# Optimization experiments

Measured on AMD Instinct MI355X. Metric: run time of the kernel, lower is better.

The kernel has to match this reference:

```python
import jax, jax.numpy as jnp
import numpy as np

ROUNDS = 2
N_NODES = 50000
N_EDGES = 800000
NODE_DIM = 128
EDGE_DIM = 32
ACT_DIM = 128


def setup_inputs() -> dict:
    key = jax.random.key(0)
    ks = jax.random.split(key, 10)
    hv = jax.random.normal(ks[0], (N_NODES, NODE_DIM), dtype=jnp.float32)
    he = jax.random.normal(ks[1], (N_EDGES, EDGE_DIM), dtype=jnp.float32)
    src = jax.random.randint(ks[2], (N_EDGES,), 0, N_NODES, dtype=jnp.int32)
    dst = jax.random.randint(ks[3], (N_EDGES,), 0, N_NODES, dtype=jnp.int32)
    cat_dim = 2 * NODE_DIM + EDGE_DIM  # 288
    W_msg = jax.random.normal(ks[4], (ROUNDS, cat_dim, ACT_DIM), dtype=jnp.float32) * 0.05
    b_msg = jax.random.normal(ks[5], (ROUNDS, ACT_DIM), dtype=jnp.float32) * 0.05
    W_ih = jax.random.normal(ks[6], (ROUNDS, ACT_DIM, 3 * NODE_DIM), dtype=jnp.float32) * 0.05
    W_hh = jax.random.normal(ks[7], (ROUNDS, NODE_DIM, 3 * NODE_DIM), dtype=jnp.float32) * 0.05
    b_ih = jax.random.normal(ks[8], (ROUNDS, 3 * NODE_DIM), dtype=jnp.float32) * 0.05
    b_hh = jax.random.normal(ks[9], (ROUNDS, 3 * NODE_DIM), dtype=jnp.float32) * 0.05
    return {"hv": hv, "he": he, "src": src, "dst": dst,
            "W_msg": W_msg, "b_msg": b_msg,
            "W_ih": W_ih, "W_hh": W_hh, "b_ih": b_ih, "b_hh": b_hh}


def _gru_cell(x, h, W_ih, W_hh, b_ih, b_hh):
    # torch.nn.GRUCell math, gate order (r, z, n)
    gi = x @ W_ih + b_ih  # [N, 3H]
    gh = h @ W_hh + b_hh  # [N, 3H]
    ir, iz, in_ = jnp.split(gi, 3, axis=-1)
    hr, hz, hn = jnp.split(gh, 3, axis=-1)
    r = jax.nn.sigmoid(ir + hr)
    z = jax.nn.sigmoid(iz + hz)
    n = jnp.tanh(in_ + r * hn)
    return (1.0 - z) * n + z * h


def reference(hv, he, src, dst, W_msg, b_msg, W_ih, W_hh, b_ih, b_hh):
    N, nd = hv.shape
    for t in range(ROUNDS):
        # Linear on concat([hv_src, hv_dst, he]) == sum of block matmuls
        Ws = W_msg[t, :nd]          # src block
        Wd = W_msg[t, nd:2 * nd]    # dst block
        We = W_msg[t, 2 * nd:]      # edge block
        msg = hv[src] @ Ws + hv[dst] @ Wd + he @ We + b_msg[t]  # [E, act]
        a = jax.ops.segment_sum(msg, dst, num_segments=N)        # per-node sum over incoming edges
        hv = _gru_cell(a, hv, W_ih[t], W_hh[t], b_ih[t], b_hh[t])
    return hv
```

## Files before the change

### kernel.cpp

```cpp
#include <hip/hip_runtime.h>

#define N_NODES 50000
#define N_EDGES 800000
#define ND 128
#define ED 32
#define AD 128
#define CAT 288
#define G3 384

#define XPAD 296
#define KSTEPS 9
#define SCAN_BS 512

typedef unsigned short ushort_t;
typedef __attribute__((ext_vector_type(8))) short bfrag;
typedef __attribute__((ext_vector_type(4))) float f32x4;

__device__ __forceinline__ unsigned int f2bf(float f) {
    unsigned int u = __float_as_uint(f);
    return (u + 0x7FFFu + ((u >> 16) & 1u)) >> 16;
}
__device__ __forceinline__ void split2(float a, float b,
                                       unsigned int& hi, unsigned int& lo) {
    const unsigned int ha = f2bf(a), hb = f2bf(b);
    const float ra = a - __uint_as_float(ha << 16);
    const float rb = b - __uint_as_float(hb << 16);
    hi = ha | (hb << 16);
    lo = f2bf(ra) | (f2bf(rb) << 16);
}
__device__ __forceinline__ void split1(float a, ushort_t& hi, ushort_t& lo) {
    const unsigned int ha = f2bf(a);
    const float ra = a - __uint_as_float(ha << 16);
    hi = (ushort_t)ha;
    lo = (ushort_t)f2bf(ra);
}

__global__ __launch_bounds__(256) void hist_kernel(
    const int* __restrict__ dst, int* __restrict__ deg)
{
    const int e = blockIdx.x * 256 + threadIdx.x;
    if (e < N_EDGES) atomicAdd(&deg[dst[e]], 1);
}

__global__ __launch_bounds__(SCAN_BS) void scan_block_kernel(
    const int* __restrict__ in, int* __restrict__ out,
    int* __restrict__ bsum, int n)
{
    __shared__ int s[SCAN_BS];
    const int g = blockIdx.x * SCAN_BS + threadIdx.x;
    const int v = (g < n) ? in[g] : 0;
    s[threadIdx.x] = v;
    __syncthreads();
    for (int off = 1; off < SCAN_BS; off <<= 1) {
        const int x = (threadIdx.x >= off) ? s[threadIdx.x - off] : 0;
        __syncthreads();
        s[threadIdx.x] += x;
        __syncthreads();
    }
    if (g < n) out[g] = s[threadIdx.x] - v;
    if (threadIdx.x == SCAN_BS - 1) bsum[blockIdx.x] = s[threadIdx.x];
}

__global__ __launch_bounds__(128) void scan_sums_kernel(int* __restrict__ bsum, int nb)
{
    __shared__ int s[128];
    const int i = threadIdx.x;
    s[i] = (i < nb) ? bsum[i] : 0;
    __syncthreads();
    if (i == 0) {
        int acc = 0;
        for (int k = 0; k < nb; ++k) { const int t = s[k]; s[k] = acc; acc += t; }
    }
    __syncthreads();
    if (i < nb) bsum[i] = s[i];
}

__global__ __launch_bounds__(SCAN_BS) void scan_add_kernel(
    int* __restrict__ rowptr, int* __restrict__ cursor,
    const int* __restrict__ bsum, int n)
{
    const int g = blockIdx.x * SCAN_BS + threadIdx.x;
    if (g < n) {
        const int v = rowptr[g] + bsum[blockIdx.x];
        rowptr[g] = v;
        cursor[g] = v;
    }
}

__global__ __launch_bounds__(256) void fill_kernel(
    const int* __restrict__ dst, const int* __restrict__ src,
    int* __restrict__ cursor, int* __restrict__ perm,
    int* __restrict__ src_sorted)
{
    const int e = blockIdx.x * 256 + threadIdx.x;
    if (e < N_EDGES) {
        const int p = atomicAdd(&cursor[dst[e]], 1);
        perm[p] = e;
        src_sorted[p] = src[e];
    }
}

__global__ __launch_bounds__(256) void esum_kernel(
    const float* __restrict__ he, const int* __restrict__ perm,
    const int* __restrict__ rowptr, float* __restrict__ E)
{
    const int id = blockIdx.x * 256 + threadIdx.x;
    if (id >= N_NODES * ED) return;
    const int v = id >> 5, c = id & 31;
    const int r0 = rowptr[v], r1 = rowptr[v + 1];
    float s = 0.f;
    int i = r0;
    for (; i + 4 <= r1; i += 4) {
        const int p0 = perm[i],     p1 = perm[i + 1];
        const int p2 = perm[i + 2], p3 = perm[i + 3];
        const float a = he[(size_t)p0 * ED + c];
        const float b = he[(size_t)p1 * ED + c];
        const float d = he[(size_t)p2 * ED + c];
        const float f = he[(size_t)p3 * ED + c];
        s += (a + b) + (d + f);
    }
    for (; i < r1; ++i)
        s += he[(size_t)perm[i] * ED + c];
    E[(size_t)v * ED + c] = s;
}

__global__ __launch_bounds__(256) void convert_w_kernel(
    const float* __restrict__ W,
    ushort_t* __restrict__ Wt_hi, ushort_t* __restrict__ Wt_lo)
{
    const int id = blockIdx.x * 256 + threadIdx.x;
    if (id >= 2 * CAT * AD) return;
    const int n = id & (AD - 1);
    const int k = (id >> 7) % CAT;
    const int t = id / (CAT * AD);
    const float w = W[(size_t)t * CAT * AD + (size_t)k * AD + n];
    const unsigned int hi = f2bf(w);
    const float r = w - __uint_as_float(hi << 16);
    const size_t o = (size_t)t * AD * CAT + (size_t)n * CAT + k;
    Wt_hi[o] = (ushort_t)hi;
    Wt_lo[o] = (ushort_t)f2bf(r);
}

__global__ __launch_bounds__(256) void convert_gatew_kernel(
    const float* __restrict__ W_ih, const float* __restrict__ W_hh,
    ushort_t* __restrict__ Bih_hi, ushort_t* __restrict__ Bih_lo,
    ushort_t* __restrict__ Bhh_hi, ushort_t* __restrict__ Bhh_lo)
{
    const int id = blockIdx.x * 256 + threadIdx.x;
    if (id >= 196608) return;
    const int t   = id / 98304;
    const int rem = id % 98304;
    const int mat = rem / 49152;
    const int q   = rem % 49152;
    const int nt = q / 2048,  r1 = q % 2048;
    const int ks = r1 / 512,  r2 = r1 % 512;
    const int kq = r2 / 128,  r3 = r2 % 128;
    const int lr = r3 / 8,    j  = r3 % 8;
    const int n = nt * 16 + lr;
    const int k = ks * 32 + kq * 8 + j;
    const float* W = mat ? W_hh : W_ih;
    const float w = W[(size_t)t * ND * G3 + (size_t)k * G3 + n];
    const unsigned int hi = f2bf(w);
    const float res = w - __uint_as_float(hi << 16);
    const size_t o = (size_t)t * 49152 + q;
    if (mat) { Bhh_hi[o] = (ushort_t)hi; Bhh_lo[o] = (ushort_t)f2bf(res); }
    else     { Bih_hi[o] = (ushort_t)hi; Bih_lo[o] = (ushort_t)f2bf(res); }
}

__global__ __launch_bounds__(256) void agg_kernel(
    const float* __restrict__ hv, const int* __restrict__ src_sorted,
    const int* __restrict__ rowptr,
    ushort_t* __restrict__ S_hi, ushort_t* __restrict__ S_lo)
{
    const int v = blockIdx.x * 4 + (threadIdx.x >> 6);
    if (v >= N_NODES) return;
    const int lane = threadIdx.x & 63;
    const int r0 = rowptr[v], r1 = rowptr[v + 1];
    const float2* hv2 = (const float2*)hv;
    float sx = 0.f, sy = 0.f;
    int i = r0;
    for (; i + 8 <= r1; i += 8) {
        const int s0 = src_sorted[i],     s1 = src_sorted[i + 1];
        const int s2 = src_sorted[i + 2], s3 = src_sorted[i + 3];
        const int s4 = src_sorted[i + 4], s5 = src_sorted[i + 5];
        const int s6 = src_sorted[i + 6], s7 = src_sorted[i + 7];
        const float2 a = hv2[(size_t)s0 * 64 + lane];
        const float2 b = hv2[(size_t)s1 * 64 + lane];
        const float2 c = hv2[(size_t)s2 * 64 + lane];
        const float2 d = hv2[(size_t)s3 * 64 + lane];
        const float2 e = hv2[(size_t)s4 * 64 + lane];
        const float2 f = hv2[(size_t)s5 * 64 + lane];
        const float2 g = hv2[(size_t)s6 * 64 + lane];
        const float2 h = hv2[(size_t)s7 * 64 + lane];
        sx += ((a.x + b.x) + (c.x + d.x)) + ((e.x + f.x) + (g.x + h.x));
        sy += ((a.y + b.y) + (c.y + d.y)) + ((e.y + f.y) + (g.y + h.y));
    }
    for (; i < r1; ++i) {
        const float2 a = hv2[(size_t)src_sorted[i] * 64 + lane];
        sx += a.x; sy += a.y;
    }
    unsigned int h, l;
    split2(sx, sy, h, l);
    ((unsigned int*)S_hi)[(size_t)v * 64 + lane] = h;
    ((unsigned int*)S_lo)[(size_t)v * 64 + lane] = l;
}

__global__ __launch_bounds__(256, 2) void fused_msg_gru_kernel(
    const ushort_t* __restrict__ S_hi, const ushort_t* __restrict__ S_lo,
    const float* __restrict__ h_cur, const float* __restrict__ E,
    const int* __restrict__ rowptr,
    const ushort_t* __restrict__ Wt_hi, const ushort_t* __restrict__ Wt_lo,
    const float* __restrict__ bmsg,
    const ushort_t* __restrict__ Bih_hi, const ushort_t* __restrict__ Bih_lo,
    const ushort_t* __restrict__ Bhh_hi, const ushort_t* __restrict__ Bhh_lo,
    const float* __restrict__ b_ih, const float* __restrict__ b_hh,
    float* __restrict__ h_out)
{
    __shared__ __align__(16) char smem[67072];
    ushort_t* xh    = (ushort_t*)smem;
    ushort_t* xl    = xh + 32 * XPAD;
    ushort_t* sh_hi = xl + 32 * XPAD;
    ushort_t* sh_lo = sh_hi + 32 * 136;
    ushort_t* sa_hi = (ushort_t*)smem;
    ushort_t* sa_lo = sa_hi + 32 * 136;
    float* grz = (float*)smem;
    float* gin = grz + 32 * 260;
    float* ghn = gin + 32 * 132;
    __shared__ float sdeg[32];

    const int t    = threadIdx.x;
    const int wave = t >> 6;
    const int lane = t & 63;
    const int kq   = lane >> 4;
    const int lr   = lane & 15;
    const int n0   = blockIdx.x * 32;

    bfrag mbh[2][KSTEPS], mbl[2][KSTEPS];
    float mbias[2];
    #pragma unroll
    for (int nt = 0; nt < 2; ++nt) {
        const int n = wave * 32 + nt * 16 + lr;
        mbias[nt] = bmsg[n];
        const ushort_t* ph = Wt_hi + (size_t)n * CAT + kq * 8;
        const ushort_t* pl = Wt_lo + (size_t)n * CAT + kq * 8;
        #pragma unroll
        for (int ks = 0; ks < KSTEPS; ++ks) {
            mbh[nt][ks] = *(const bfrag*)(ph + ks * 32);
            mbl[nt][ks] = *(const bfrag*)(pl + ks * 32);
        }
    }

    {
        const int row = t >> 3, c8 = t & 7;
        const int n = min(n0 + row, N_NODES - 1);
        if (t < 32) {
            const int nn = min(n0 + t, N_NODES - 1);
            sdeg[t] = (float)(rowptr[nn + 1] - rowptr[nn]);
        }
        {
            const uint4* ph = (const uint4*)(S_hi + (size_t)n * ND + c8 * 16);
            const uint4* pl = (const uint4*)(S_lo + (size_t)n * ND + c8 * 16);
            *(uint4*)&xh[row * XPAD + c8 * 16]     = ph[0];
            *(uint4*)&xh[row * XPAD + c8 * 16 + 8] = ph[1];
            *(uint4*)&xl[row * XPAD + c8 * 16]     = pl[0];
            *(uint4*)&xl[row * XPAD + c8 * 16 + 8] = pl[1];
        }
        {
            const float degf = (float)(rowptr[n + 1] - rowptr[n]);
            const float4* hp = (const float4*)(h_cur + (size_t)n * ND + c8 * 16);
            const float4 v0 = hp[0], v1 = hp[1], v2 = hp[2], v3 = hp[3];
            uint4 h0, h1, l0, l1;
            split2(v0.x, v0.y, h0.x, l0.x); split2(v0.z, v0.w, h0.y, l0.y);
            split2(v1.x, v1.y, h0.z, l0.z); split2(v1.z, v1.w, h0.w, l0.w);
            split2(v2.x, v2.y, h1.x, l1.x); split2(v2.z, v2.w, h1.y, l1.y);
            split2(v3.x, v3.y, h1.z, l1.z); split2(v3.z, v3.w, h1.w, l1.w);
            const int so = row * 136 + c8 * 16;
            *(uint4*)(sh_hi + so) = h0;  *(uint4*)(sh_hi + so + 8) = h1;
            *(uint4*)(sh_lo + so) = l0;  *(uint4*)(sh_lo + so + 8) = l1;
            uint4 g0, g1, m0, m1;
            split2(v0.x * degf, v0.y * degf, g0.x, m0.x); split2(v0.z * degf, v0.w * degf, g0.y, m0.y);
            split2(v1.x * degf, v1.y * degf, g0.z, m0.z); split2(v1.z * degf, v1.w * degf, g0.w, m0.w);
            split2(v2.x * degf, v2.y * degf, g1.x, m1.x); split2(v2.z * degf, v2.w * degf, g1.y, m1.y);
            split2(v3.x * degf, v3.y * degf, g1.z, m1.z); split2(v3.z * degf, v3.w * degf, g1.w, m1.w);
            *(uint4*)&xh[row * XPAD + ND + c8 * 16]     = g0;
            *(uint4*)&xh[row * XPAD + ND + c8 * 16 + 8] = g1;
            *(uint4*)&xl[row * XPAD + ND + c8 * 16]     = m0;
            *(uint4*)&xl[row * XPAD + ND + c8 * 16 + 8] = m1;
        }
        {
            const float4 e4 = *(const float4*)(E + (size_t)n * ED + c8 * 4);
            uint2 h0, l0;
            split2(e4.x, e4.y, h0.x, l0.x); split2(e4.z, e4.w, h0.y, l0.y);
            *(uint2*)&xh[row * XPAD + 2 * ND + c8 * 4] = h0;
            *(uint2*)&xl[row * XPAD + 2 * ND + c8 * 4] = l0;
        }
    }
    __syncthreads();

    f32x4 acc00 = {0.f,0.f,0.f,0.f}, acc01 = {0.f,0.f,0.f,0.f};
    f32x4 acc10 = {0.f,0.f,0.f,0.f}, acc11 = {0.f,0.f,0.f,0.f};
    #pragma unroll
    for (int ks = 0; ks < KSTEPS; ++ks) {
        const int ko = ks * 32 + kq * 8;
        const bfrag a0h = *(const bfrag*)&xh[lr * XPAD + ko];
        const bfrag a0l = *(const bfrag*)&xl[lr * XPAD + ko];
        const bfrag a1h = *(const bfrag*)&xh[(16 + lr) * XPAD + ko];
        const bfrag a1l = *(const bfrag*)&xl[(16 + lr) * XPAD + ko];
        acc00 = __builtin_amdgcn_mfma_f32_16x16x32_bf16(a0h, mbh[0][ks], acc00, 0, 0, 0);
        acc00 = __builtin_amdgcn_mfma_f32_16x16x32_bf16(a0l, mbh[0][ks], acc00, 0, 0, 0);
        acc00 = __builtin_amdgcn_mfma_f32_16x16x32_bf16(a0h, mbl[0][ks], acc00, 0, 0, 0);
        acc01 = __builtin_amdgcn_mfma_f32_16x16x32_bf16(a0h, mbh[1][ks], acc01, 0, 0, 0);
        acc01 = __builtin_amdgcn_mfma_f32_16x16x32_bf16(a0l, mbh[1][ks], acc01, 0, 0, 0);
        acc01 = __builtin_amdgcn_mfma_f32_16x16x32_bf16(a0h, mbl[1][ks], acc01, 0, 0, 0);
        acc10 = __builtin_amdgcn_mfma_f32_16x16x32_bf16(a1h, mbh[0][ks], acc10, 0, 0, 0);
        acc10 = __builtin_amdgcn_mfma_f32_16x16x32_bf16(a1l, mbh[0][ks], acc10, 0, 0, 0);
        acc10 = __builtin_amdgcn_mfma_f32_16x16x32_bf16(a1h, mbl[0][ks], acc10, 0, 0, 0);
        acc11 = __builtin_amdgcn_mfma_f32_16x16x32_bf16(a1h, mbh[1][ks], acc11, 0, 0, 0);
        acc11 = __builtin_amdgcn_mfma_f32_16x16x32_bf16(a1l, mbh[1][ks], acc11, 0, 0, 0);
        acc11 = __builtin_amdgcn_mfma_f32_16x16x32_bf16(a1h, mbl[1][ks], acc11, 0, 0, 0);
    }
    __syncthreads();

    #pragma unroll
    for (int r = 0; r < 4; ++r) {
        const int row0 = kq * 4 + r;
        const int row1 = 16 + kq * 4 + r;
        const int c0 = wave * 32 + lr, c1 = wave * 32 + 16 + lr;
        ushort_t h, l;
        split1(acc00[r] + sdeg[row0] * mbias[0], h, l);
        sa_hi[row0 * 136 + c0] = h; sa_lo[row0 * 136 + c0] = l;
        split1(acc01[r] + sdeg[row0] * mbias[1], h, l);
        sa_hi[row0 * 136 + c1] = h; sa_lo[row0 * 136 + c1] = l;
        split1(acc10[r] + sdeg[row1] * mbias[0], h, l);
        sa_hi[row1 * 136 + c0] = h; sa_lo[row1 * 136 + c0] = l;
        split1(acc11[r] + sdeg[row1] * mbias[1], h, l);
        sa_hi[row1 * 136 + c1] = h; sa_lo[row1 * 136 + c1] = l;
    }
    __syncthreads();

    f32x4 acc_i[2][6], acc_h[2][6];
    #pragma unroll
    for (int m = 0; m < 2; ++m)
        #pragma unroll
        for (int nt = 0; nt < 6; ++nt) {
            acc_i[m][nt] = (f32x4){0.f, 0.f, 0.f, 0.f};
            acc_h[m][nt] = (f32x4){0.f, 0.f, 0.f, 0.f};
        }

    #pragma unroll
    for (int ks = 0; ks < 4; ++ks) {
        bfrag afh[2], afl[2], hfh[2], hfl[2];
        #pragma unroll
        for (int m = 0; m < 2; ++m) {
            const int ao = (m * 16 + lr) * 136 + ks * 32 + kq * 8;
            afh[m] = *(const bfrag*)(sa_hi + ao);
            afl[m] = *(const bfrag*)(sa_lo + ao);
            hfh[m] = *(const bfrag*)(sh_hi + ao);
            hfl[m] = *(const bfrag*)(sh_lo + ao);
        }
        #pragma unroll
        for (int nt = 0; nt < 6; ++nt) {
            const int gnt = wave * 6 + nt;
            const int bo = (((gnt * 4 + ks) * 4 + kq) * 16 + lr) * 8;
            const bfrag bih_h = *(const bfrag*)(Bih_hi + bo);
            const bfrag bih_l = *(const bfrag*)(Bih_lo + bo);
            const bfrag bhh_h = *(const bfrag*)(Bhh_hi + bo);
            const bfrag bhh_l = *(const bfrag*)(Bhh_lo + bo);
            #pragma unroll
            for (int m = 0; m < 2; ++m) {
                acc_i[m][nt] = __builtin_amdgcn_mfma_f32_16x16x32_bf16(afh[m], bih_h, acc_i[m][nt], 0, 0, 0);
                acc_i[m][nt] = __builtin_amdgcn_mfma_f32_16x16x32_bf16(afl[m], bih_h, acc_i[m][nt], 0, 0, 0);
                acc_i[m][nt] = __builtin_amdgcn_mfma_f32_16x16x32_bf16(afh[m], bih_l, acc_i[m][nt], 0, 0, 0);
                acc_h[m][nt] = __builtin_amdgcn_mfma_f32_16x16x32_bf16(hfh[m], bhh_h, acc_h[m][nt], 0, 0, 0);
                acc_h[m][nt] = __builtin_amdgcn_mfma_f32_16x16x32_bf16(hfl[m], bhh_h, acc_h[m][nt], 0, 0, 0);
                acc_h[m][nt] = __builtin_amdgcn_mfma_f32_16x16x32_bf16(hfh[m], bhh_l, acc_h[m][nt], 0, 0, 0);
            }
        }
    }
    __syncthreads();

    #pragma unroll
    for (int nt = 0; nt < 6; ++nt) {
        const int gcol = wave * 96 + nt * 16 + lr;
        if (gcol < 256) {
            const float bias = b_ih[gcol] + b_hh[gcol];
            #pragma unroll
            for (int m = 0; m < 2; ++m)
                #pragma unroll
                for (int r = 0; r < 4; ++r)
                    grz[(m * 16 + kq * 4 + r) * 260 + gcol] =
                        acc_i[m][nt][r] + acc_h[m][nt][r] + bias;
        } else {
            const int cc = gcol - 256;
            const float bi = b_ih[gcol], bh2 = b_hh[gcol];
            #pragma unroll
            for (int m = 0; m < 2; ++m)
                #pragma unroll
                for (int r = 0; r < 4; ++r) {
                    const int rw = m * 16 + kq * 4 + r;
                    gin[rw * 132 + cc] = acc_i[m][nt][r] + bi;
                    ghn[rw * 132 + cc] = acc_h[m][nt][r] + bh2;
                }
        }
    }
    __syncthreads();

    for (int idx = t; idx < 32 * ND; idx += 256) {
        const int nl = idx >> 7, cc = idx & 127;
        const int n = n0 + nl;
        if (n < N_NODES) {
            const float rp  = grz[nl * 260 + cc];
            const float zp  = grz[nl * 260 + 128 + cc];
            const float inp = gin[nl * 132 + cc];
            const float hnp = ghn[nl * 132 + cc];
            const float r = 1.f / (1.f + expf(-rp));
            const float z = 1.f / (1.f + expf(-zp));
            const float nn = tanhf(inp + r * hnp);
            h_out[(size_t)n * ND + cc] =
                (1.f - z) * nn + z * h_cur[(size_t)n * ND + cc];
        }
    }
}

extern "C" void kernel_launch(void* const* d_in, const int* in_sizes, int n_in,
                              void* d_out, int out_size, void* d_ws, size_t ws_size,
                              hipStream_t stream)
{
    const float* hv   = (const float*)d_in[0];
    const float* he   = (const float*)d_in[1];
    const int*   src  = (const int*)d_in[2];
    const int*   dst  = (const int*)d_in[3];
    const float* Wmsg = (const float*)d_in[4];
    const float* bmsg = (const float*)d_in[5];
    const float* Wih  = (const float*)d_in[6];
    const float* Whh  = (const float*)d_in[7];
    const float* bih  = (const float*)d_in[8];
    const float* bhh  = (const float*)d_in[9];
    float* out = (float*)d_out;

    const int nscan = ((N_NODES + SCAN_BS - 1) / SCAN_BS) * SCAN_BS;
    const int nblk  = nscan / SCAN_BS;

    char* p = (char*)d_ws;
    ushort_t* S_hi = (ushort_t*)p;            p += (size_t)N_NODES * ND * 2;
    ushort_t* S_lo = (ushort_t*)p;            p += (size_t)N_NODES * ND * 2;
    float* E = (float*)p;                     p += (size_t)N_NODES * ED * 4;
    ushort_t* Wt_hi = (ushort_t*)p;           p += (size_t)2 * AD * CAT * 2;
    ushort_t* Wt_lo = (ushort_t*)p;           p += (size_t)2 * AD * CAT * 2;
    ushort_t* Bih_hi = (ushort_t*)p;          p += (size_t)2 * G3 * ND * 2;
    ushort_t* Bih_lo = (ushort_t*)p;          p += (size_t)2 * G3 * ND * 2;
    ushort_t* Bhh_hi = (ushort_t*)p;          p += (size_t)2 * G3 * ND * 2;
    ushort_t* Bhh_lo = (ushort_t*)p;          p += (size_t)2 * G3 * ND * 2;
    int* deg    = (int*)p;                    p += (size_t)nscan * 4;
    int* rowptr = (int*)p;                    p += (size_t)nscan * 4;
    int* cursor = (int*)p;                    p += (size_t)nscan * 4;
    int* bsum   = (int*)p;                    p += 128 * 4;
    int* perm   = (int*)p;                    p += (size_t)N_EDGES * 4;
    int* src_sorted = (int*)p;                p += (size_t)N_EDGES * 4;

    convert_w_kernel<<<(2 * CAT * AD + 255) / 256, 256, 0, stream>>>(Wmsg, Wt_hi, Wt_lo);
    convert_gatew_kernel<<<768, 256, 0, stream>>>(Wih, Whh, Bih_hi, Bih_lo, Bhh_hi, Bhh_lo);

    hipMemsetAsync(deg, 0, (size_t)nscan * 4, stream);
    hist_kernel<<<(N_EDGES + 255) / 256, 256, 0, stream>>>(dst, deg);
    scan_block_kernel<<<nblk, SCAN_BS, 0, stream>>>(deg, rowptr, bsum, nscan);
    scan_sums_kernel<<<1, 128, 0, stream>>>(bsum, nblk);
    scan_add_kernel<<<nblk, SCAN_BS, 0, stream>>>(rowptr, cursor, bsum, nscan);
    fill_kernel<<<(N_EDGES + 255) / 256, 256, 0, stream>>>(dst, src, cursor, perm, src_sorted);
    esum_kernel<<<(N_NODES * ED + 255) / 256, 256, 0, stream>>>(he, perm, rowptr, E);

    const int tile_blocks = (N_NODES + 31) / 32;

    for (int t = 0; t < 2; ++t) {
        const float* h_cur = (t == 0) ? hv : out;
        agg_kernel<<<(N_NODES + 3) / 4, 256, 0, stream>>>(
            h_cur, src_sorted, rowptr, S_hi, S_lo);
        fused_msg_gru_kernel<<<tile_blocks, 256, 0, stream>>>(
            S_hi, S_lo, h_cur, E, rowptr,
            Wt_hi + (size_t)t * AD * CAT, Wt_lo + (size_t)t * AD * CAT,
            bmsg + (size_t)t * AD,
            Bih_hi + (size_t)t * G3 * ND, Bih_lo + (size_t)t * G3 * ND,
            Bhh_hi + (size_t)t * G3 * ND, Bhh_lo + (size_t)t * G3 * ND,
            bih + (size_t)t * G3, bhh + (size_t)t * G3, out);
    }
}
```

Measured before the change: 584.3 us.

## Fuse neighbor aggregation into the per-round message/GRU kernel

Drops the separate aggregation kernel and its bf16 hi/lo intermediate. Each block now gathers and sums neighbor hidden rows for its 32-node tile directly into shared memory. The message weights move to a fragment-packed layout read from global memory instead of being held in registers, and the degree scaling of h_dst is applied to a separate accumulator rather than to the inputs. The GRU epilogue runs straight from the MFMA accumulators without a shared-memory staging pass, and occupancy rises to 3 blocks. The cost is that the irregular gather now runs inside a register-heavy kernel with less parallelism per node (8 threads per node instead of a wave), and a ping-pong buffer is added so round 2 does not read rows it is overwriting.

```diff
diff --git a/kernel.cpp b/kernel.cpp
--- a/kernel.cpp
+++ b/kernel.cpp
@@ -126,19 +126,24 @@
 
 __global__ __launch_bounds__(256) void convert_w_kernel(
     const float* __restrict__ W,
-    ushort_t* __restrict__ Wt_hi, ushort_t* __restrict__ Wt_lo)
+    ushort_t* __restrict__ Wm_hi, ushort_t* __restrict__ Wm_lo)
 {
     const int id = blockIdx.x * 256 + threadIdx.x;
-    if (id >= 2 * CAT * AD) return;
-    const int n = id & (AD - 1);
-    const int k = (id >> 7) % CAT;
-    const int t = id / (CAT * AD);
+    if (id >= 2 * 36864) return;
+    const int t = id / 36864;
+    const int q = id % 36864;
+    const int nt = q / 4608,  r1 = q % 4608;
+    const int ks = r1 / 512,  r2 = r1 % 512;
+    const int kq = r2 / 128,  r3 = r2 % 128;
+    const int lr = r3 / 8,    j  = r3 % 8;
+    const int n = nt * 16 + lr;
+    const int k = ks * 32 + kq * 8 + j;
     const float w = W[(size_t)t * CAT * AD + (size_t)k * AD + n];
     const unsigned int hi = f2bf(w);
     const float r = w - __uint_as_float(hi << 16);
-    const size_t o = (size_t)t * AD * CAT + (size_t)n * CAT + k;
-    Wt_hi[o] = (ushort_t)hi;
-    Wt_lo[o] = (ushort_t)f2bf(r);
+    const size_t o = (size_t)t * 36864 + q;
+    Wm_hi[o] = (ushort_t)hi;
+    Wm_lo[o] = (ushort_t)f2bf(r);
 }
 
 __global__ __launch_bounds__(256) void convert_gatew_kernel(
@@ -167,65 +172,18 @@
     else     { Bih_hi[o] = (ushort_t)hi; Bih_lo[o] = (ushort_t)f2bf(res); }
 }
 
-__global__ __launch_bounds__(256) void agg_kernel(
-    const float* __restrict__ hv, const int* __restrict__ src_sorted,
-    const int* __restrict__ rowptr,
-    ushort_t* __restrict__ S_hi, ushort_t* __restrict__ S_lo)
-{
-    const int v = blockIdx.x * 4 + (threadIdx.x >> 6);
-    if (v >= N_NODES) return;
-    const int lane = threadIdx.x & 63;
-    const int r0 = rowptr[v], r1 = rowptr[v + 1];
-    const float2* hv2 = (const float2*)hv;
-    float sx = 0.f, sy = 0.f;
-    int i = r0;
-    for (; i + 8 <= r1; i += 8) {
-        const int s0 = src_sorted[i],     s1 = src_sorted[i + 1];
-        const int s2 = src_sorted[i + 2], s3 = src_sorted[i + 3];
-        const int s4 = src_sorted[i + 4], s5 = src_sorted[i + 5];
-        const int s6 = src_sorted[i + 6], s7 = src_sorted[i + 7];
-        const float2 a = hv2[(size_t)s0 * 64 + lane];
-        const float2 b = hv2[(size_t)s1 * 64 + lane];
-        const float2 c = hv2[(size_t)s2 * 64 + lane];
-        const float2 d = hv2[(size_t)s3 * 64 + lane];
-        const float2 e = hv2[(size_t)s4 * 64 + lane];
-        const float2 f = hv2[(size_t)s5 * 64 + lane];
-        const float2 g = hv2[(size_t)s6 * 64 + lane];
-        const float2 h = hv2[(size_t)s7 * 64 + lane];
-        sx += ((a.x + b.x) + (c.x + d.x)) + ((e.x + f.x) + (g.x + h.x));
-        sy += ((a.y + b.y) + (c.y + d.y)) + ((e.y + f.y) + (g.y + h.y));
-    }
-    for (; i < r1; ++i) {
-        const float2 a = hv2[(size_t)src_sorted[i] * 64 + lane];
-        sx += a.x; sy += a.y;
-    }
-    unsigned int h, l;
-    split2(sx, sy, h, l);
-    ((unsigned int*)S_hi)[(size_t)v * 64 + lane] = h;
-    ((unsigned int*)S_lo)[(size_t)v * 64 + lane] = l;
-}
-
-__global__ __launch_bounds__(256, 2) void fused_msg_gru_kernel(
-    const ushort_t* __restrict__ S_hi, const ushort_t* __restrict__ S_lo,
+__global__ __launch_bounds__(256, 3) void fused_round_kernel(
     const float* __restrict__ h_cur, const float* __restrict__ E,
-    const int* __restrict__ rowptr,
-    const ushort_t* __restrict__ Wt_hi, const ushort_t* __restrict__ Wt_lo,
+    const int* __restrict__ rowptr, const int* __restrict__ src_sorted,
+    const ushort_t* __restrict__ Wm_hi, const ushort_t* __restrict__ Wm_lo,
     const float* __restrict__ bmsg,
     const ushort_t* __restrict__ Bih_hi, const ushort_t* __restrict__ Bih_lo,
     const ushort_t* __restrict__ Bhh_hi, const ushort_t* __restrict__ Bhh_lo,
     const float* __restrict__ b_ih, const float* __restrict__ b_hh,
     float* __restrict__ h_out)
 {
-    __shared__ __align__(16) char smem[67072];
-    ushort_t* xh    = (ushort_t*)smem;
-    ushort_t* xl    = xh + 32 * XPAD;
-    ushort_t* sh_hi = xl + 32 * XPAD;
-    ushort_t* sh_lo = sh_hi + 32 * 136;
-    ushort_t* sa_hi = (ushort_t*)smem;
-    ushort_t* sa_lo = sa_hi + 32 * 136;
-    float* grz = (float*)smem;
-    float* gin = grz + 32 * 260;
-    float* ghn = gin + 32 * 132;
+    __shared__ ushort_t xh[32 * XPAD];
+    __shared__ ushort_t xl[32 * XPAD];
     __shared__ float sdeg[32];
 
     const int t    = threadIdx.x;
@@ -235,70 +193,78 @@
     const int lr   = lane & 15;
     const int n0   = blockIdx.x * 32;
 
-    bfrag mbh[2][KSTEPS], mbl[2][KSTEPS];
+    {
+        const int nr = t >> 3, cg = t & 7;
+        const int n  = min(n0 + nr, N_NODES - 1);
+        const int r0 = rowptr[n], r1 = rowptr[n + 1];
+        if (cg == 0) sdeg[nr] = (float)(r1 - r0);
+
+        float4 s0 = {0,0,0,0}, s1 = {0,0,0,0}, s2 = {0,0,0,0}, s3 = {0,0,0,0};
+        const float4* hv4 = (const float4*)h_cur;
+        int i = r0;
+        for (; i + 2 <= r1; i += 2) {
+            const int sa = src_sorted[i], sb = src_sorted[i + 1];
+            const float4* pa = hv4 + (size_t)sa * 32 + cg * 4;
+            const float4* pb = hv4 + (size_t)sb * 32 + cg * 4;
+            const float4 a0 = pa[0], a1 = pa[1], a2 = pa[2], a3 = pa[3];
+            const float4 b0 = pb[0], b1 = pb[1], b2 = pb[2], b3 = pb[3];
+            s0.x += a0.x + b0.x; s0.y += a0.y + b0.y; s0.z += a0.z + b0.z; s0.w += a0.w + b0.w;
+            s1.x += a1.x + b1.x; s1.y += a1.y + b1.y; s1.z += a1.z + b1.z; s1.w += a1.w + b1.w;
+            s2.x += a2.x + b2.x; s2.y += a2.y + b2.y; s2.z += a2.z + b2.z; s2.w += a2.w + b2.w;
+            s3.x += a3.x + b3.x; s3.y += a3.y + b3.y; s3.z += a3.z + b3.z; s3.w += a3.w + b3.w;
+        }
+        if (i < r1) {
+            const float4* pa = hv4 + (size_t)src_sorted[i] * 32 + cg * 4;
+            const float4 a0 = pa[0], a1 = pa[1], a2 = pa[2], a3 = pa[3];
+            s0.x += a0.x; s0.y += a0.y; s0.z += a0.z; s0.w += a0.w;
+            s1.x += a1.x; s1.y += a1.y; s1.z += a1.z; s1.w += a1.w;
+            s2.x += a2.x; s2.y += a2.y; s2.z += a2.z; s2.w += a2.w;
+            s3.x += a3.x; s3.y += a3.y; s3.z += a3.z; s3.w += a3.w;
+        }
+        uint4 H0, L0, H1, L1;
+        split2(s0.x, s0.y, H0.x, L0.x); split2(s0.z, s0.w, H0.y, L0.y);
+        split2(s1.x, s1.y, H0.z, L0.z); split2(s1.z, s1.w, H0.w, L0.w);
+        split2(s2.x, s2.y, H1.x, L1.x); split2(s2.z, s2.w, H1.y, L1.y);
+        split2(s3.x, s3.y, H1.z, L1.z); split2(s3.z, s3.w, H1.w, L1.w);
+        *(uint4*)&xh[nr * XPAD + cg * 16]     = H0;
+        *(uint4*)&xh[nr * XPAD + cg * 16 + 8] = H1;
+        *(uint4*)&xl[nr * XPAD + cg * 16]     = L0;
+        *(uint4*)&xl[nr * XPAD + cg * 16 + 8] = L1;
+
+        {
+            const float4* hp = (const float4*)(h_cur + (size_t)n * ND + cg * 16);
+            const float4 v0 = hp[0], v1 = hp[1], v2 = hp[2], v3 = hp[3];
+            split2(v0.x, v0.y, H0.x, L0.x); split2(v0.z, v0.w, H0.y, L0.y);
+            split2(v1.x, v1.y, H0.z, L0.z); split2(v1.z, v1.w, H0.w, L0.w);
+            split2(v2.x, v2.y, H1.x, L1.x); split2(v2.z, v2.w, H1.y, L1.y);
+            split2(v3.x, v3.y, H1.z, L1.z); split2(v3.z, v3.w, H1.w, L1.w);
+            *(uint4*)&xh[nr * XPAD + ND + cg * 16]     = H0;
+            *(uint4*)&xh[nr * XPAD + ND + cg * 16 + 8] = H1;
+            *(uint4*)&xl[nr * XPAD + ND + cg * 16]     = L0;
+            *(uint4*)&xl[nr * XPAD + ND + cg * 16 + 8] = L1;
+        }
+        {
+            const float4 e4 = *(const float4*)(E + (size_t)n * ED + cg * 4);
+            uint2 h2, l2;
+            split2(e4.x, e4.y, h2.x, l2.x); split2(e4.z, e4.w, h2.y, l2.y);
+            *(uint2*)&xh[nr * XPAD + 2 * ND + cg * 4] = h2;
+            *(uint2*)&xl[nr * XPAD + 2 * ND + cg * 4] = l2;
+        }
+    }
+    __syncthreads();
+
+    f32x4 aS[2][2], aH[2][2];
+    #pragma unroll
+    for (int m = 0; m < 2; ++m)
+        #pragma unroll
+        for (int nt = 0; nt < 2; ++nt) {
+            aS[m][nt] = (f32x4){0.f, 0.f, 0.f, 0.f};
+            aH[m][nt] = (f32x4){0.f, 0.f, 0.f, 0.f};
+        }
     float mbias[2];
     #pragma unroll
-    for (int nt = 0; nt < 2; ++nt) {
-        const int n = wave * 32 + nt * 16 + lr;
-        mbias[nt] = bmsg[n];
-        const ushort_t* ph = Wt_hi + (size_t)n * CAT + kq * 8;
-        const ushort_t* pl = Wt_lo + (size_t)n * CAT + kq * 8;
-        #pragma unroll
-        for (int ks = 0; ks < KSTEPS; ++ks) {
-            mbh[nt][ks] = *(const bfrag*)(ph + ks * 32);
-            mbl[nt][ks] = *(const bfrag*)(pl + ks * 32);
-        }
-    }
-
-    {
-        const int row = t >> 3, c8 = t & 7;
-        const int n = min(n0 + row, N_NODES - 1);
-        if (t < 32) {
-            const int nn = min(n0 + t, N_NODES - 1);
-            sdeg[t] = (float)(rowptr[nn + 1] - rowptr[nn]);
-        }
-        {
-            const uint4* ph = (const uint4*)(S_hi + (size_t)n * ND + c8 * 16);
-            const uint4* pl = (const uint4*)(S_lo + (size_t)n * ND + c8 * 16);
-            *(uint4*)&xh[row * XPAD + c8 * 16]     = ph[0];
-            *(uint4*)&xh[row * XPAD + c8 * 16 + 8] = ph[1];
-            *(uint4*)&xl[row * XPAD + c8 * 16]     = pl[0];
-            *(uint4*)&xl[row * XPAD + c8 * 16 + 8] = pl[1];
-        }
-        {
-            const float degf = (float)(rowptr[n + 1] - rowptr[n]);
-            const float4* hp = (const float4*)(h_cur + (size_t)n * ND + c8 * 16);
-            const float4 v0 = hp[0], v1 = hp[1], v2 = hp[2], v3 = hp[3];
-            uint4 h0, h1, l0, l1;
-            split2(v0.x, v0.y, h0.x, l0.x); split2(v0.z, v0.w, h0.y, l0.y);
-            split2(v1.x, v1.y, h0.z, l0.z); split2(v1.z, v1.w, h0.w, l0.w);
-            split2(v2.x, v2.y, h1.x, l1.x); split2(v2.z, v2.w, h1.y, l1.y);
-            split2(v3.x, v3.y, h1.z, l1.z); split2(v3.z, v3.w, h1.w, l1.w);
-            const int so = row * 136 + c8 * 16;
-            *(uint4*)(sh_hi + so) = h0;  *(uint4*)(sh_hi + so + 8) = h1;
-            *(uint4*)(sh_lo + so) = l0;  *(uint4*)(sh_lo + so + 8) = l1;
-            uint4 g0, g1, m0, m1;
-            split2(v0.x * degf, v0.y * degf, g0.x, m0.x); split2(v0.z * degf, v0.w * degf, g0.y, m0.y);
-            split2(v1.x * degf, v1.y * degf, g0.z, m0.z); split2(v1.z * degf, v1.w * degf, g0.w, m0.w);
-            split2(v2.x * degf, v2.y * degf, g1.x, m1.x); split2(v2.z * degf, v2.w * degf, g1.y, m1.y);
-            split2(v3.x * degf, v3.y * degf, g1.z, m1.z); split2(v3.z * degf, v3.w * degf, g1.w, m1.w);
-            *(uint4*)&xh[row * XPAD + ND + c8 * 16]     = g0;
-            *(uint4*)&xh[row * XPAD + ND + c8 * 16 + 8] = g1;
-            *(uint4*)&xl[row * XPAD + ND + c8 * 16]     = m0;
-            *(uint4*)&xl[row * XPAD + ND + c8 * 16 + 8] = m1;
-        }
-        {
-            const float4 e4 = *(const float4*)(E + (size_t)n * ED + c8 * 4);
-            uint2 h0, l0;
-            split2(e4.x, e4.y, h0.x, l0.x); split2(e4.z, e4.w, h0.y, l0.y);
-            *(uint2*)&xh[row * XPAD + 2 * ND + c8 * 4] = h0;
-            *(uint2*)&xl[row * XPAD + 2 * ND + c8 * 4] = l0;
-        }
-    }
-    __syncthreads();
-
-    f32x4 acc00 = {0.f,0.f,0.f,0.f}, acc01 = {0.f,0.f,0.f,0.f};
-    f32x4 acc10 = {0.f,0.f,0.f,0.f}, acc11 = {0.f,0.f,0.f,0.f};
+    for (int nt = 0; nt < 2; ++nt) mbias[nt] = bmsg[wave * 32 + nt * 16 + lr];
+
     #pragma unroll
     for (int ks = 0; ks < KSTEPS; ++ks) {
         const int ko = ks * 32 + kq * 8;
@@ -306,35 +272,46 @@
         const bfrag a0l = *(const bfrag*)&xl[lr * XPAD + ko];
         const bfrag a1h = *(const bfrag*)&xh[(16 + lr) * XPAD + ko];
         const bfrag a1l = *(const bfrag*)&xl[(16 + lr) * XPAD + ko];
-        acc00 = __builtin_amdgcn_mfma_f32_16x16x32_bf16(a0h, mbh[0][ks], acc00, 0, 0, 0);
-        acc00 = __builtin_amdgcn_mfma_f32_16x16x32_bf16(a0l, mbh[0][ks], acc00, 0, 0, 0);
-        acc00 = __builtin_amdgcn_mfma_f32_16x16x32_bf16(a0h, mbl[0][ks], acc00, 0, 0, 0);
-        acc01 = __builtin_amdgcn_mfma_f32_16x16x32_bf16(a0h, mbh[1][ks], acc01, 0, 0, 0);
-        acc01 = __builtin_amdgcn_mfma_f32_16x16x32_bf16(a0l, mbh[1][ks], acc01, 0, 0, 0);
-        acc01 = __builtin_amdgcn_mfma_f32_16x16x32_bf16(a0h, mbl[1][ks], acc01, 0, 0, 0);
-        acc10 = __builtin_amdgcn_mfma_f32_16x16x32_bf16(a1h, mbh[0][ks], acc10, 0, 0, 0);
-        acc10 = __builtin_amdgcn_mfma_f32_16x16x32_bf16(a1l, mbh[0][ks], acc10, 0, 0, 0);
-        acc10 = __builtin_amdgcn_mfma_f32_16x16x32_bf16(a1h, mbl[0][ks], acc10, 0, 0, 0);
-        acc11 = __builtin_amdgcn_mfma_f32_16x16x32_bf16(a1h, mbh[1][ks], acc11, 0, 0, 0);
-        acc11 = __builtin_amdgcn_mfma_f32_16x16x32_bf16(a1l, mbh[1][ks], acc11, 0, 0, 0);
-        acc11 = __builtin_amdgcn_mfma_f32_16x16x32_bf16(a1h, mbl[1][ks], acc11, 0, 0, 0);
-    }
-    __syncthreads();
-
-    #pragma unroll
-    for (int r = 0; r < 4; ++r) {
-        const int row0 = kq * 4 + r;
-        const int row1 = 16 + kq * 4 + r;
-        const int c0 = wave * 32 + lr, c1 = wave * 32 + 16 + lr;
-        ushort_t h, l;
-        split1(acc00[r] + sdeg[row0] * mbias[0], h, l);
-        sa_hi[row0 * 136 + c0] = h; sa_lo[row0 * 136 + c0] = l;
-        split1(acc01[r] + sdeg[row0] * mbias[1], h, l);
-        sa_hi[row0 * 136 + c1] = h; sa_lo[row0 * 136 + c1] = l;
-        split1(acc10[r] + sdeg[row1] * mbias[0], h, l);
-        sa_hi[row1 * 136 + c0] = h; sa_lo[row1 * 136 + c0] = l;
-        split1(acc11[r] + sdeg[row1] * mbias[1], h, l);
-        sa_hi[row1 * 136 + c1] = h; sa_lo[row1 * 136 + c1] = l;
+        const size_t b0 = ((((size_t)(wave * 2 + 0) * 9 + ks) * 4 + kq) * 16 + lr) * 8;
+        const size_t b1 = ((((size_t)(wave * 2 + 1) * 9 + ks) * 4 + kq) * 16 + lr) * 8;
+        const bfrag w0h = *(const bfrag*)(Wm_hi + b0);
+        const bfrag w0l = *(const bfrag*)(Wm_lo + b0);
+        const bfrag w1h = *(const bfrag*)(Wm_hi + b1);
+        const bfrag w1l = *(const bfrag*)(Wm_lo + b1);
+        auto step = [&](f32x4 (&acc)[2][2]) {
+            acc[0][0] = __builtin_amdgcn_mfma_f32_16x16x32_bf16(a0h, w0h, acc[0][0], 0, 0, 0);
+            acc[0][0] = __builtin_amdgcn_mfma_f32_16x16x32_bf16(a0l, w0h, acc[0][0], 0, 0, 0);
+            acc[0][0] = __builtin_amdgcn_mfma_f32_16x16x32_bf16(a0h, w0l, acc[0][0], 0, 0, 0);
+            acc[0][1] = __builtin_amdgcn_mfma_f32_16x16x32_bf16(a0h, w1h, acc[0][1], 0, 0, 0);
+            acc[0][1] = __builtin_amdgcn_mfma_f32_16x16x32_bf16(a0l, w1h, acc[0][1], 0, 0, 0);
+            acc[0][1] = __builtin_amdgcn_mfma_f32_16x16x32_bf16(a0h, w1l, acc[0][1], 0, 0, 0);
+            acc[1][0] = __builtin_amdgcn_mfma_f32_16x16x32_bf16(a1h, w0h, acc[1][0], 0, 0, 0);
+            acc[1][0] = __builtin_amdgcn_mfma_f32_16x16x32_bf16(a1l, w0h, acc[1][0], 0, 0, 0);
+            acc[1][0] = __builtin_amdgcn_mfma_f32_16x16x32_bf16(a1h, w0l, acc[1][0], 0, 0, 0);
+            acc[1][1] = __builtin_amdgcn_mfma_f32_16x16x32_bf16(a1h, w1h, acc[1][1], 0, 0, 0);
+            acc[1][1] = __builtin_amdgcn_mfma_f32_16x16x32_bf16(a1l, w1h, acc[1][1], 0, 0, 0);
+            acc[1][1] = __builtin_amdgcn_mfma_f32_16x16x32_bf16(a1h, w1l, acc[1][1], 0, 0, 0);
+        };
+        if (ks >= 4 && ks < 8) step(aH); else step(aS);
+    }
+    __syncthreads();
+
+    #pragma unroll
+    for (int m = 0; m < 2; ++m) {
+        #pragma unroll
+        for (int r = 0; r < 4; ++r) {
+            const int row = m * 16 + kq * 4 + r;
+            const float degf = sdeg[row];
+            #pragma unroll
+            for (int nt = 0; nt < 2; ++nt) {
+                const int c = wave * 32 + nt * 16 + lr;
+                const float v = aS[m][nt][r] + degf * (aH[m][nt][r] + mbias[nt]);
+                ushort_t h, l;
+                split1(v, h, l);
+                xh[row * XPAD + c] = h;
+                xl[row * XPAD + c] = l;
+            }
+        }
     }
     __syncthreads();
 
@@ -342,9 +319,9 @@
     #pragma unroll
     for (int m = 0; m < 2; ++m)
         #pragma unroll
-        for (int nt = 0; nt < 6; ++nt) {
-            acc_i[m][nt] = (f32x4){0.f, 0.f, 0.f, 0.f};
-            acc_h[m][nt] = (f32x4){0.f, 0.f, 0.f, 0.f};
+        for (int g = 0; g < 6; ++g) {
+            acc_i[m][g] = (f32x4){0.f, 0.f, 0.f, 0.f};
+            acc_h[m][g] = (f32x4){0.f, 0.f, 0.f, 0.f};
         }
 
     #pragma unroll
@@ -352,72 +329,57 @@
         bfrag afh[2], afl[2], hfh[2], hfl[2];
         #pragma unroll
         for (int m = 0; m < 2; ++m) {
-            const int ao = (m * 16 + lr) * 136 + ks * 32 + kq * 8;
-            afh[m] = *(const bfrag*)(sa_hi + ao);
-            afl[m] = *(const bfrag*)(sa_lo + ao);
-            hfh[m] = *(const bfrag*)(sh_hi + ao);
-            hfl[m] = *(const bfrag*)(sh_lo + ao);
-        }
-        #pragma unroll
-        for (int nt = 0; nt < 6; ++nt) {
-            const int gnt = wave * 6 + nt;
-            const int bo = (((gnt * 4 + ks) * 4 + kq) * 16 + lr) * 8;
+            const int ao = (m * 16 + lr) * XPAD + ks * 32 + kq * 8;
+            afh[m] = *(const bfrag*)&xh[ao];
+            afl[m] = *(const bfrag*)&xl[ao];
+            hfh[m] = *(const bfrag*)&xh[ao + ND];
+            hfl[m] = *(const bfrag*)&xl[ao + ND];
+        }
+        #pragma unroll
+        for (int lnt = 0; lnt < 6; ++lnt) {
+            const int gnt = (lnt >> 1) * 8 + wave * 2 + (lnt & 1);
+            const size_t bo = ((((size_t)gnt * 4 + ks) * 4 + kq) * 16 + lr) * 8;
             const bfrag bih_h = *(const bfrag*)(Bih_hi + bo);
             const bfrag bih_l = *(const bfrag*)(Bih_lo + bo);
             const bfrag bhh_h = *(const bfrag*)(Bhh_hi + bo);
             const bfrag bhh_l = *(const bfrag*)(Bhh_lo + bo);
             #pragma unroll
             for (int m = 0; m < 2; ++m) {
-                acc_i[m][nt] = __builtin_amdgcn_mfma_f32_16x16x32_bf16(afh[m], bih_h, acc_i[m][nt], 0, 0, 0);
-                acc_i[m][nt] = __builtin_amdgcn_mfma_f32_16x16x32_bf16(afl[m], bih_h, acc_i[m][nt], 0, 0, 0);
-                acc_i[m][nt] = __builtin_amdgcn_mfma_f32_16x16x32_bf16(afh[m], bih_l, acc_i[m][nt], 0, 0, 0);
-                acc_h[m][nt] = __builtin_amdgcn_mfma_f32_16x16x32_bf16(hfh[m], bhh_h, acc_h[m][nt], 0, 0, 0);
-                acc_h[m][nt] = __builtin_amdgcn_mfma_f32_16x16x32_bf16(hfl[m], bhh_h, acc_h[m][nt], 0, 0, 0);
-                acc_h[m][nt] = __builtin_amdgcn_mfma_f32_16x16x32_bf16(hfh[m], bhh_l, acc_h[m][nt], 0, 0, 0);
+                acc_i[m][lnt] = __builtin_amdgcn_mfma_f32_16x16x32_bf16(afh[m], bih_h, acc_i[m][lnt], 0, 0, 0);
+                acc_i[m][lnt] = __builtin_amdgcn_mfma_f32_16x16x32_bf16(afl[m], bih_h, acc_i[m][lnt], 0, 0, 0);
+                acc_i[m][lnt] = __builtin_amdgcn_mfma_f32_16x16x32_bf16(afh[m], bih_l, acc_i[m][lnt], 0, 0, 0);
+                acc_h[m][lnt] = __builtin_amdgcn_mfma_f32_16x16x32_bf16(hfh[m], bhh_h, acc_h[m][lnt], 0, 0, 0);
+                acc_h[m][lnt] = __builtin_amdgcn_mfma_f32_16x16x32_bf16(hfl[m], bhh_h, acc_h[m][lnt], 0, 0, 0);
+                acc_h[m][lnt] = __builtin_amdgcn_mfma_f32_16x16x32_bf16(hfh[m], bhh_l, acc_h[m][lnt], 0, 0, 0);
             }
         }
     }
-    __syncthreads();
-
-    #pragma unroll
-    for (int nt = 0; nt < 6; ++nt) {
-        const int gcol = wave * 96 + nt * 16 + lr;
-        if (gcol < 256) {
-            const float bias = b_ih[gcol] + b_hh[gcol];
+
+    #pragma unroll
+    for (int j = 0; j < 2; ++j) {
+        const int cj = wave * 32 + j * 16 + lr;
+        const float bir = b_ih[cj],       bhr = b_hh[cj];
+        const float biz = b_ih[128 + cj], bhz = b_hh[128 + cj];
+        const float bin = b_ih[256 + cj], bhn = b_hh[256 + cj];
+        #pragma unroll
+        for (int m = 0; m < 2; ++m) {
             #pragma unroll
-            for (int m = 0; m < 2; ++m)
-                #pragma unroll
-                for (int r = 0; r < 4; ++r)
-                    grz[(m * 16 + kq * 4 + r) * 260 + gcol] =
-                        acc_i[m][nt][r] + acc_h[m][nt][r] + bias;
-        } else {
-            const int cc = gcol - 256;
-            const float bi = b_ih[gcol], bh2 = b_hh[gcol];
-            #pragma unroll
-            for (int m = 0; m < 2; ++m)
-                #pragma unroll
-                for (int r = 0; r < 4; ++r) {
-                    const int rw = m * 16 + kq * 4 + r;
-                    gin[rw * 132 + cc] = acc_i[m][nt][r] + bi;
-                    ghn[rw * 132 + cc] = acc_h[m][nt][r] + bh2;
-                }
-        }
-    }
-    __syncthreads();
-
-    for (int idx = t; idx < 32 * ND; idx += 256) {
-        const int nl = idx >> 7, cc = idx & 127;
-        const int n = n0 + nl;
-        if (n < N_NODES) {
-            const float rp  = grz[nl * 260 + cc];
-            const float zp  = grz[nl * 260 + 128 + cc];
-            const float inp = gin[nl * 132 + cc];
-            const float hnp = ghn[nl * 132 + cc];
-            const float r = 1.f / (1.f + expf(-rp));
-            const float z = 1.f / (1.f + expf(-zp));
-            const float nn = tanhf(inp + r * hnp);
-            h_out[(size_t)n * ND + cc] =
-                (1.f - z) * nn + z * h_cur[(size_t)n * ND + cc];
+            for (int r = 0; r < 4; ++r) {
+                const int row = m * 16 + kq * 4 + r;
+                const int node = n0 + row;
+                const float rp  = acc_i[m][0 + j][r] + acc_h[m][0 + j][r] + bir + bhr;
+                const float zp  = acc_i[m][2 + j][r] + acc_h[m][2 + j][r] + biz + bhz;
+                const float inp = acc_i[m][4 + j][r] + bin;
+                const float hnp = acc_h[m][4 + j][r] + bhn;
+                const float rg = 1.f / (1.f + expf(-rp));
+                const float z  = 1.f / (1.f + expf(-zp));
+                const float nn = tanhf(inp + rg * hnp);
+                const unsigned int hh = xh[row * XPAD + ND + cj];
+                const unsigned int hl = xl[row * XPAD + ND + cj];
+                const float hval = __uint_as_float(hh << 16) + __uint_as_float(hl << 16);
+                if (node < N_NODES)
+                    h_out[(size_t)node * ND + cj] = (1.f - z) * nn + z * hval;
+            }
         }
     }
 }
@@ -442,11 +404,10 @@
     const int nblk  = nscan / SCAN_BS;
 
     char* p = (char*)d_ws;
-    ushort_t* S_hi = (ushort_t*)p;            p += (size_t)N_NODES * ND * 2;
-    ushort_t* S_lo = (ushort_t*)p;            p += (size_t)N_NODES * ND * 2;
+    float* h_tmp = (float*)p;                 p += (size_t)N_NODES * ND * 4;
     float* E = (float*)p;                     p += (size_t)N_NODES * ED * 4;
-    ushort_t* Wt_hi = (ushort_t*)p;           p += (size_t)2 * AD * CAT * 2;
-    ushort_t* Wt_lo = (ushort_t*)p;           p += (size_t)2 * AD * CAT * 2;
+    ushort_t* Wm_hi = (ushort_t*)p;           p += (size_t)2 * 36864 * 2;
+    ushort_t* Wm_lo = (ushort_t*)p;           p += (size_t)2 * 36864 * 2;
     ushort_t* Bih_hi = (ushort_t*)p;          p += (size_t)2 * G3 * ND * 2;
     ushort_t* Bih_lo = (ushort_t*)p;          p += (size_t)2 * G3 * ND * 2;
     ushort_t* Bhh_hi = (ushort_t*)p;          p += (size_t)2 * G3 * ND * 2;
@@ -458,7 +419,7 @@
     int* perm   = (int*)p;                    p += (size_t)N_EDGES * 4;
     int* src_sorted = (int*)p;                p += (size_t)N_EDGES * 4;
 
-    convert_w_kernel<<<(2 * CAT * AD + 255) / 256, 256, 0, stream>>>(Wmsg, Wt_hi, Wt_lo);
+    convert_w_kernel<<<(2 * 36864 + 255) / 256, 256, 0, stream>>>(Wmsg, Wm_hi, Wm_lo);
     convert_gatew_kernel<<<768, 256, 0, stream>>>(Wih, Whh, Bih_hi, Bih_lo, Bhh_hi, Bhh_lo);
 
     hipMemsetAsync(deg, 0, (size_t)nscan * 4, stream);
@@ -472,15 +433,14 @@
     const int tile_blocks = (N_NODES + 31) / 32;
 
     for (int t = 0; t < 2; ++t) {
-        const float* h_cur = (t == 0) ? hv : out;
-        agg_kernel<<<(N_NODES + 3) / 4, 256, 0, stream>>>(
-            h_cur, src_sorted, rowptr, S_hi, S_lo);
-        fused_msg_gru_kernel<<<tile_blocks, 256, 0, stream>>>(
-            S_hi, S_lo, h_cur, E, rowptr,
-            Wt_hi + (size_t)t * AD * CAT, Wt_lo + (size_t)t * AD * CAT,
+        const float* h_cur = (t == 0) ? hv : h_tmp;
+        float* h_dst       = (t == 0) ? h_tmp : out;
+        fused_round_kernel<<<tile_blocks, 256, 0, stream>>>(
+            h_cur, E, rowptr, src_sorted,
+            Wm_hi + (size_t)t * 36864, Wm_lo + (size_t)t * 36864,
             bmsg + (size_t)t * AD,
             Bih_hi + (size_t)t * G3 * ND, Bih_lo + (size_t)t * G3 * ND,
             Bhh_hi + (size_t)t * G3 * ND, Bhh_lo + (size_t)t * G3 * ND,
-            bih + (size_t)t * G3, bhh + (size_t)t * G3, out);
-    }
-}
+            bih + (size_t)t * G3, bhh + (size_t)t * G3, h_dst);
+    }
+}
```

After: 618.0 us. +5.8%, slower.
